# Performance work log

Hardware: AMD Instinct MI355X
Metric: run time of the kernel (lower is better)

## Reference

```python
import jax, jax.numpy as jnp
import numpy as np

N_NODES = 50000
IN_CH = 256
HID_CH = 64
N_EDGES = 800000


def setup_inputs() -> dict:
    key = jax.random.key(0)
    k1, k2, k3, k4, k5 = jax.random.split(key, 5)
    x = jax.random.normal(k1, (N_NODES, IN_CH), dtype=jnp.float32)
    edge_index = jax.random.randint(k2, (2, N_EDGES), 0, N_NODES, dtype=jnp.int64)
    # GCNConv linear weight (Glorot) and zero bias, as in PyG defaults
    W = jax.random.normal(k3, (IN_CH, HID_CH), dtype=jnp.float32) * (1.0 / np.sqrt(IN_CH))
    bias = jnp.zeros((HID_CH,), dtype=jnp.float32)
    # PReLU per-channel weight, torch default init 0.25
    prelu_a = jnp.full((HID_CH,), 0.25, dtype=jnp.float32)
    return {"x": x, "edge_index": edge_index, "W": W, "bias": bias, "prelu_a": prelu_a}


def reference(x, edge_index, W, bias, prelu_a):
    # GCNConv, normalize=False: transform then scatter-add over edges, + bias
    xw = x @ W                               # [N, H]
    src, dst = edge_index[0], edge_index[1]
    msgs = xw[src]                           # [E, H] gather
    agg = jax.ops.segment_sum(msgs, dst, num_segments=N_NODES)  # [N, H]
    out = agg + bias
    # per-channel PReLU
    return jnp.where(out > 0, out, prelu_a * out)
```

## Files before the change

### kernel.cpp

```cpp
#include <hip/hip_runtime.h>

#define N_NODES 50000
#define IN_CH   256
#define HID_CH  64
#define N_EDGES 800000

#define AG_ROWS 64
#define NBUCKET 782
#define CAPB    1536
#define PTILE   4096
#define NPT     196
#define GEMM_BLOCKS 391
#define CAP     2048

typedef __attribute__((ext_vector_type(8))) short short8;
typedef __attribute__((ext_vector_type(4))) float f32x4;

static __device__ __forceinline__ float bf2f(unsigned short h) {
    return __uint_as_float(((unsigned int)h) << 16);
}
static __device__ __forceinline__ unsigned int cvt_pk(float lo, float hi) {
    unsigned int r;
    asm("v_cvt_pk_bf16_f32 %0, %1, %2" : "=v"(r) : "v"(lo), "v"(hi));
    return r;
}

union SmemU {
    short8 wfl[2048];
    struct {
        int hcnt[NBUCKET];
        int excl[NBUCKET];
        int lcur[NBUCKET];
        int gbase[NBUCKET];
        int wsum[8];
        unsigned int staged[PTILE];
        unsigned short sbkt[PTILE];
    } p;
};

__global__ __launch_bounds__(512, 4) void gemm_part_kernel(const float* __restrict__ x,
                                                           const float* __restrict__ W,
                                                           unsigned short* __restrict__ xwb,
                                                           const int* __restrict__ ei,
                                                           int* __restrict__ cnt,
                                                           unsigned int* __restrict__ packed_out) {
    __shared__ SmemU u;
    const int t = threadIdx.x;
    const int bid = blockIdx.x;

    int pid = -1, gid = -1;
    if ((bid & 1) && (bid >> 1) < NPT) pid = bid >> 1;
    else gid = (bid < 2 * NPT) ? (bid >> 1) : (bid - NPT);

    if (gid >= 0) {
        for (int e = t; e < 2048; e += 512) {
            const int ks = e >> 8;
            const int nt = (e >> 6) & 3;
            const int l  = e & 63;
            const int q = l >> 4, m = l & 15;
            const int n = nt * 16 + m;
            const int k0 = ks * 32 + q * 8;
            const float* wp = W + (size_t)k0 * HID_CH + n;
            uint4 v;
            v.x = cvt_pk(wp[0 * HID_CH], wp[1 * HID_CH]);
            v.y = cvt_pk(wp[2 * HID_CH], wp[3 * HID_CH]);
            v.z = cvt_pk(wp[4 * HID_CH], wp[5 * HID_CH]);
            v.w = cvt_pk(wp[6 * HID_CH], wp[7 * HID_CH]);
            ((uint4*)u.wfl)[e] = v;
        }
        __syncthreads();

        const int wv = t >> 6, lane = t & 63;
        const int q = lane >> 4, m = lane & 15;
        const int row0 = gid * 128 + wv * 16;
        const int arow = row0 + m;
        const int arl = arow < N_NODES ? arow : N_NODES - 1;
        const float* xr = x + (size_t)arl * IN_CH + q * 8;

        float4 areg[16];
        #pragma unroll
        for (int ks = 0; ks < 8; ++ks) {
            areg[2 * ks]     = *(const float4*)(xr + ks * 32);
            areg[2 * ks + 1] = *(const float4*)(xr + ks * 32 + 4);
        }

        f32x4 acc0 = {0.f,0.f,0.f,0.f}, acc1 = acc0, acc2 = acc0, acc3 = acc0;

        #pragma unroll
        for (int ks = 0; ks < 8; ++ks) {
            short8 af;
            unsigned int* afu = (unsigned int*)&af;
            afu[0] = cvt_pk(areg[2 * ks].x,     areg[2 * ks].y);
            afu[1] = cvt_pk(areg[2 * ks].z,     areg[2 * ks].w);
            afu[2] = cvt_pk(areg[2 * ks + 1].x, areg[2 * ks + 1].y);
            afu[3] = cvt_pk(areg[2 * ks + 1].z, areg[2 * ks + 1].w);
            const short8 b0 = u.wfl[(ks * 4 + 0) * 64 + lane];
            const short8 b1 = u.wfl[(ks * 4 + 1) * 64 + lane];
            const short8 b2 = u.wfl[(ks * 4 + 2) * 64 + lane];
            const short8 b3 = u.wfl[(ks * 4 + 3) * 64 + lane];
            acc0 = __builtin_amdgcn_mfma_f32_16x16x32_bf16(af, b0, acc0, 0, 0, 0);
            acc1 = __builtin_amdgcn_mfma_f32_16x16x32_bf16(af, b1, acc1, 0, 0, 0);
            acc2 = __builtin_amdgcn_mfma_f32_16x16x32_bf16(af, b2, acc2, 0, 0, 0);
            acc3 = __builtin_amdgcn_mfma_f32_16x16x32_bf16(af, b3, acc3, 0, 0, 0);
        }

        #pragma unroll
        for (int r = 0; r < 4; ++r) {
            const int row = row0 + q * 4 + r;
            if (row < N_NODES) {
                unsigned short* o = xwb + (size_t)row * HID_CH + m;
                const unsigned int p01 = cvt_pk(acc0[r], acc1[r]);
                const unsigned int p23 = cvt_pk(acc2[r], acc3[r]);
                o[0]  = (unsigned short)(p01 & 0xFFFFu);
                o[16] = (unsigned short)(p01 >> 16);
                o[32] = (unsigned short)(p23 & 0xFFFFu);
                o[48] = (unsigned short)(p23 >> 16);
            }
        }
        return;
    }

    const int tile0 = pid * PTILE;
    const int tcnt = min(PTILE, N_EDGES - tile0);

    for (int i = t; i < NBUCKET; i += 512) u.p.hcnt[i] = 0;
    __syncthreads();

    int es[8], ed[8];
    #pragma unroll
    for (int r = 0; r < 2; ++r) {
        const int base = tile0 + (r * 512 + t) * 4;
        if (base < N_EDGES) {
            const int4 s4 = *(const int4*)(ei + base);
            const int4 d4 = *(const int4*)(ei + N_EDGES + base);
            es[r*4+0] = s4.x; es[r*4+1] = s4.y; es[r*4+2] = s4.z; es[r*4+3] = s4.w;
            ed[r*4+0] = d4.x; ed[r*4+1] = d4.y; ed[r*4+2] = d4.z; ed[r*4+3] = d4.w;
        } else {
            #pragma unroll
            for (int j = 0; j < 4; ++j) es[r*4+j] = -1;
        }
    }
    #pragma unroll
    for (int i = 0; i < 8; ++i)
        if (es[i] >= 0) atomicAdd(&u.p.hcnt[ed[i] >> 6], 1);
    __syncthreads();

    const int b0 = 2 * t, b1 = 2 * t + 1;
    const int c0 = (b0 < NBUCKET) ? u.p.hcnt[b0] : 0;
    const int c1 = (b1 < NBUCKET) ? u.p.hcnt[b1] : 0;
    const int v = c0 + c1;
    int s = v;
    #pragma unroll
    for (int off = 1; off < 64; off <<= 1) {
        const int uu = __shfl_up(s, off, 64);
        if ((t & 63) >= off) s += uu;
    }
    if ((t & 63) == 63) u.p.wsum[t >> 6] = s;
    __syncthreads();
    if (t < 8) {
        const int ws = u.p.wsum[t];
        int si = ws;
        #pragma unroll
        for (int off = 1; off < 8; off <<= 1) {
            const int uu = __shfl_up(si, off, 64);
            if (t >= off) si += uu;
        }
        u.p.wsum[t] = si - ws;
    }
    __syncthreads();
    const int ex = s - v + u.p.wsum[t >> 6];
    if (b0 < NBUCKET) {
        u.p.excl[b0] = ex; u.p.lcur[b0] = ex;
        if (c0 > 0) u.p.gbase[b0] = b0 * CAPB + atomicAdd(&cnt[b0], c0);
    }
    if (b1 < NBUCKET) {
        u.p.excl[b1] = ex + c0; u.p.lcur[b1] = ex + c0;
        if (c1 > 0) u.p.gbase[b1] = b1 * CAPB + atomicAdd(&cnt[b1], c1);
    }
    __syncthreads();

    #pragma unroll
    for (int i = 0; i < 8; ++i) {
        if (es[i] >= 0) {
            const int b = ed[i] >> 6;
            const int pos = atomicAdd(&u.p.lcur[b], 1);
            u.p.staged[pos] = ((unsigned int)(ed[i] & 63) << 16) | (unsigned int)es[i];
            u.p.sbkt[pos] = (unsigned short)b;
        }
    }
    __syncthreads();

    #pragma unroll
    for (int i = 0; i < 8; ++i) {
        const int idx = t + i * 512;
        if (idx < tcnt) {
            const int b = u.p.sbkt[idx];
            packed_out[u.p.gbase[b] + (idx - u.p.excl[b])] = u.p.staged[idx];
        }
    }
}

__global__ __launch_bounds__(512) void aggregate_kernel(const unsigned short* __restrict__ xwb,
                                                        const unsigned int* __restrict__ packed,
                                                        const int* __restrict__ cnt,
                                                        const float* __restrict__ bias,
                                                        const float* __restrict__ prelu_a,
                                                        float* __restrict__ out) {
    __shared__ unsigned short ssrc[CAP];
    __shared__ int hcnt[AG_ROWS];
    __shared__ int hexcl[AG_ROWS];
    __shared__ int hcur[AG_ROWS];

    const int b = blockIdx.x;
    const int t = threadIdx.x;
    const int beg = b * CAPB;
    const int total = min(cnt[b], CAP);

    if (t < AG_ROWS) hcnt[t] = 0;
    __syncthreads();

    for (int i = t; i < total; i += 512)
        atomicAdd(&hcnt[packed[beg + i] >> 16], 1);
    __syncthreads();

    if (t < AG_ROWS) {
        const int v = hcnt[t];
        int s = v;
        #pragma unroll
        for (int off = 1; off < 64; off <<= 1) {
            const int u = __shfl_up(s, off, 64);
            if (t >= off) s += u;
        }
        hexcl[t] = s - v;
        hcur[t]  = s - v;
    }
    __syncthreads();

    for (int i = t; i < total; i += 512) {
        const unsigned int p = packed[beg + i];
        const int pos = atomicAdd(&hcur[p >> 16], 1);
        ssrc[pos] = (unsigned short)(p & 0xFFFFu);
    }
    __syncthreads();

    const int sl = t >> 3;
    const int li = t & 7;
    const int c0 = li * 8;
    const int rb = hexcl[sl];
    const int re = rb + hcnt[sl];

    float a[8];
    #pragma unroll
    for (int j = 0; j < 8; ++j) a[j] = 0.f;

    int i = rb;
    for (; i + 7 < re; i += 8) {
        short8 vv[8];
        #pragma unroll
        for (int r = 0; r < 8; ++r) {
            const int e = ssrc[i + r];
            vv[r] = *(const short8*)(xwb + (size_t)e * HID_CH + c0);
        }
        #pragma unroll
        for (int r = 0; r < 8; ++r)
            #pragma unroll
            for (int j = 0; j < 8; ++j)
                a[j] += bf2f((unsigned short)vv[r][j]);
    }
    for (; i + 3 < re; i += 4) {
        short8 vv[4];
        #pragma unroll
        for (int r = 0; r < 4; ++r) {
            const int e = ssrc[i + r];
            vv[r] = *(const short8*)(xwb + (size_t)e * HID_CH + c0);
        }
        #pragma unroll
        for (int r = 0; r < 4; ++r)
            #pragma unroll
            for (int j = 0; j < 8; ++j)
                a[j] += bf2f((unsigned short)vv[r][j]);
    }
    for (; i < re; ++i) {
        const int e0 = ssrc[i];
        const short8 v0 = *(const short8*)(xwb + (size_t)e0 * HID_CH + c0);
        #pragma unroll
        for (int j = 0; j < 8; ++j) a[j] += bf2f((unsigned short)v0[j]);
    }

    const int node = b * AG_ROWS + sl;
    if (node < N_NODES) {
        const float4 bb0 = *(const float4*)(bias + c0);
        const float4 bb1 = *(const float4*)(bias + c0 + 4);
        const float4 aa0 = *(const float4*)(prelu_a + c0);
        const float4 aa1 = *(const float4*)(prelu_a + c0 + 4);
        float4 r0, r1;
        r0.x = a[0] + bb0.x; r0.x = r0.x > 0.f ? r0.x : aa0.x * r0.x;
        r0.y = a[1] + bb0.y; r0.y = r0.y > 0.f ? r0.y : aa0.y * r0.y;
        r0.z = a[2] + bb0.z; r0.z = r0.z > 0.f ? r0.z : aa0.z * r0.z;
        r0.w = a[3] + bb0.w; r0.w = r0.w > 0.f ? r0.w : aa0.w * r0.w;
        r1.x = a[4] + bb1.x; r1.x = r1.x > 0.f ? r1.x : aa1.x * r1.x;
        r1.y = a[5] + bb1.y; r1.y = r1.y > 0.f ? r1.y : aa1.y * r1.y;
        r1.z = a[6] + bb1.z; r1.z = r1.z > 0.f ? r1.z : aa1.z * r1.z;
        r1.w = a[7] + bb1.w; r1.w = r1.w > 0.f ? r1.w : aa1.w * r1.w;
        float4* op = (float4*)(out + (size_t)node * HID_CH + c0);
        op[0] = r0;
        op[1] = r1;
    }
}

extern "C" void kernel_launch(void* const* d_in, const int* in_sizes, int n_in,
                              void* d_out, int out_size, void* d_ws, size_t ws_size,
                              hipStream_t stream) {
    const float* x       = (const float*)d_in[0];
    const int*   ei      = (const int*)d_in[1];
    const float* W       = (const float*)d_in[2];
    const float* bias    = (const float*)d_in[3];
    const float* prelu_a = (const float*)d_in[4];
    float* out = (float*)d_out;

    char* w = (char*)d_ws;
    unsigned short* xwb    = (unsigned short*)(w);
    int*            cnt    = (int*)(w + 6400000);
    unsigned int*   packed = (unsigned int*)(w + 6403200);

    hipMemsetAsync(cnt, 0, NBUCKET * sizeof(int), stream);

    gemm_part_kernel<<<GEMM_BLOCKS + NPT, 512, 0, stream>>>(x, W, xwb, ei, cnt, packed);

    aggregate_kernel<<<NBUCKET, 512, 0, stream>>>(xwb, packed, cnt, bias, prelu_a, out);
}
```

Baseline: 125.2 us.

## Stream GEMM x tiles through double-buffered LDS via async global_load_lds

Replaces the per-thread register preload of the full x row slice with a double-buffered LDS pipeline. It loads 32-column chunks of a 128-row tile using global_load_lds and prefetches the next chunk while computing MFMAs on the current one. The goal is to cut register pressure and overlap global loads with compute. In exchange it adds a block-wide barrier per K step and doubles the shared-memory union size to 64KB. That larger footprint can lower occupancy for both GEMM and partition blocks.

```diff
diff --git a/kernel.cpp b/kernel.cpp
--- a/kernel.cpp
+++ b/kernel.cpp
@@ -12,6 +12,7 @@
 #define NPT     196
 #define GEMM_BLOCKS 391
 #define CAP     2048
+#define XCH     32
 
 typedef __attribute__((ext_vector_type(8))) short short8;
 typedef __attribute__((ext_vector_type(4))) float f32x4;
@@ -24,9 +25,17 @@
     asm("v_cvt_pk_bf16_f32 %0, %1, %2" : "=v"(r) : "v"(lo), "v"(hi));
     return r;
 }
+typedef const __attribute__((address_space(1))) unsigned int* gas_ptr;
+typedef __attribute__((address_space(3))) unsigned int* las_ptr;
+static __device__ __forceinline__ void gl2lds16(const float* g, float* l) {
+    __builtin_amdgcn_global_load_lds((gas_ptr)(g), (las_ptr)(l), 16, 0, 0);
+}
 
 union SmemU {
-    short8 wfl[2048];
+    struct {
+        short8 wfl[2048];
+        float  xs[2][128 * XCH];
+    } g;
     struct {
         int hcnt[NBUCKET];
         int excl[NBUCKET];
@@ -53,60 +62,81 @@
     else gid = (bid < 2 * NPT) ? (bid >> 1) : (bid - NPT);
 
     if (gid >= 0) {
+        const int wv = t >> 6, lane = t & 63;
+        const int q = lane >> 4, m = lane & 15;
+        const int row0 = gid * 128;
+
+        {
+            #pragma unroll
+            for (int r = 0; r < 2; ++r) {
+                const int i = r * 512 + t;
+                const int row = i >> 3;
+                const int grow = min(row0 + row, N_NODES - 1);
+                const float* gp = x + (size_t)grow * IN_CH + 0 * XCH + (i & 7) * 4;
+                float* lp = &u.g.xs[0][(r * 512 + wv * 64) * 4];
+                gl2lds16(gp, lp);
+            }
+        }
+
         for (int e = t; e < 2048; e += 512) {
             const int ks = e >> 8;
             const int nt = (e >> 6) & 3;
             const int l  = e & 63;
-            const int q = l >> 4, m = l & 15;
-            const int n = nt * 16 + m;
-            const int k0 = ks * 32 + q * 8;
+            const int ql = l >> 4, ml = l & 15;
+            const int n = nt * 16 + ml;
+            const int k0 = ks * 32 + ql * 8;
             const float* wp = W + (size_t)k0 * HID_CH + n;
             uint4 v;
             v.x = cvt_pk(wp[0 * HID_CH], wp[1 * HID_CH]);
             v.y = cvt_pk(wp[2 * HID_CH], wp[3 * HID_CH]);
             v.z = cvt_pk(wp[4 * HID_CH], wp[5 * HID_CH]);
             v.w = cvt_pk(wp[6 * HID_CH], wp[7 * HID_CH]);
-            ((uint4*)u.wfl)[e] = v;
+            ((uint4*)u.g.wfl)[e] = v;
         }
         __syncthreads();
 
-        const int wv = t >> 6, lane = t & 63;
-        const int q = lane >> 4, m = lane & 15;
-        const int row0 = gid * 128 + wv * 16;
-        const int arow = row0 + m;
-        const int arl = arow < N_NODES ? arow : N_NODES - 1;
-        const float* xr = x + (size_t)arl * IN_CH + q * 8;
-
-        float4 areg[16];
-        #pragma unroll
-        for (int ks = 0; ks < 8; ++ks) {
-            areg[2 * ks]     = *(const float4*)(xr + ks * 32);
-            areg[2 * ks + 1] = *(const float4*)(xr + ks * 32 + 4);
-        }
-
         f32x4 acc0 = {0.f,0.f,0.f,0.f}, acc1 = acc0, acc2 = acc0, acc3 = acc0;
 
         #pragma unroll
-        for (int ks = 0; ks < 8; ++ks) {
+        for (int kc = 0; kc < 8; ++kc) {
+            const int cur = kc & 1;
+            if (kc < 7) {
+                #pragma unroll
+                for (int r = 0; r < 2; ++r) {
+                    const int i = r * 512 + t;
+                    const int row = i >> 3;
+                    const int grow = min(row0 + row, N_NODES - 1);
+                    const float* gp = x + (size_t)grow * IN_CH + (kc + 1) * XCH + (i & 7) * 4;
+                    float* lp = &u.g.xs[cur ^ 1][(r * 512 + wv * 64) * 4];
+                    gl2lds16(gp, lp);
+                }
+            }
+
+            const float* ap = &u.g.xs[cur][(wv * 16 + m) * XCH + q * 8];
+            const float4 a0 = *(const float4*)ap;
+            const float4 a1 = *(const float4*)(ap + 4);
             short8 af;
             unsigned int* afu = (unsigned int*)&af;
-            afu[0] = cvt_pk(areg[2 * ks].x,     areg[2 * ks].y);
-            afu[1] = cvt_pk(areg[2 * ks].z,     areg[2 * ks].w);
-            afu[2] = cvt_pk(areg[2 * ks + 1].x, areg[2 * ks + 1].y);
-            afu[3] = cvt_pk(areg[2 * ks + 1].z, areg[2 * ks + 1].w);
-            const short8 b0 = u.wfl[(ks * 4 + 0) * 64 + lane];
-            const short8 b1 = u.wfl[(ks * 4 + 1) * 64 + lane];
-            const short8 b2 = u.wfl[(ks * 4 + 2) * 64 + lane];
-            const short8 b3 = u.wfl[(ks * 4 + 3) * 64 + lane];
+            afu[0] = cvt_pk(a0.x, a0.y);
+            afu[1] = cvt_pk(a0.z, a0.w);
+            afu[2] = cvt_pk(a1.x, a1.y);
+            afu[3] = cvt_pk(a1.z, a1.w);
+            const short8 b0 = u.g.wfl[(kc * 4 + 0) * 64 + lane];
+            const short8 b1 = u.g.wfl[(kc * 4 + 1) * 64 + lane];
+            const short8 b2 = u.g.wfl[(kc * 4 + 2) * 64 + lane];
+            const short8 b3 = u.g.wfl[(kc * 4 + 3) * 64 + lane];
             acc0 = __builtin_amdgcn_mfma_f32_16x16x32_bf16(af, b0, acc0, 0, 0, 0);
             acc1 = __builtin_amdgcn_mfma_f32_16x16x32_bf16(af, b1, acc1, 0, 0, 0);
             acc2 = __builtin_amdgcn_mfma_f32_16x16x32_bf16(af, b2, acc2, 0, 0, 0);
             acc3 = __builtin_amdgcn_mfma_f32_16x16x32_bf16(af, b3, acc3, 0, 0, 0);
-        }
-
+
+            if (kc < 7) __syncthreads();
+        }
+
+        const int rowt = row0 + wv * 16;
         #pragma unroll
         for (int r = 0; r < 4; ++r) {
-            const int row = row0 + q * 4 + r;
+            const int row = rowt + q * 4 + r;
             if (row < N_NODES) {
                 unsigned short* o = xwb + (size_t)row * HID_CH + m;
                 const unsigned int p01 = cvt_pk(acc0[r], acc1[r]);
```

New measurement: 126.7 us. Within noise of the previous version (+1.3%).

## Fuse GEMM/partition and aggregation into one cooperative persistent kernel

Applied to the files above, without the earlier changes.

Merges the two kernels into a single cooperative kernel that loops over GEMM and partition work items, does a grid-wide sync, then loops over aggregation buckets. The aim is to drop the second kernel launch and the gap between dependent launches. In exchange the grid is capped (at most 512 blocks) and work is serialized within persistent blocks. The grid barrier also adds its own cost, and the shared-memory union grows to hold the aggregation buffers.

```diff
diff --git a/kernel.cpp b/kernel.cpp
--- a/kernel.cpp
+++ b/kernel.cpp
@@ -1,4 +1,5 @@
 #include <hip/hip_runtime.h>
+#include <hip/hip_cooperative_groups.h>
 
 #define N_NODES 50000
 #define IN_CH   256
@@ -11,6 +12,7 @@
 #define PTILE   4096
 #define NPT     196
 #define GEMM_BLOCKS 391
+#define NITEMS  (GEMM_BLOCKS + NPT)
 #define CAP     2048
 
 typedef __attribute__((ext_vector_type(8))) short short8;
@@ -36,90 +38,90 @@
         unsigned int staged[PTILE];
         unsigned short sbkt[PTILE];
     } p;
+    struct {
+        unsigned short ssrc[CAP];
+        int hcnt[AG_ROWS];
+        int hexcl[AG_ROWS];
+        int hcur[AG_ROWS];
+    } a;
 };
 
-__global__ __launch_bounds__(512, 4) void gemm_part_kernel(const float* __restrict__ x,
-                                                           const float* __restrict__ W,
-                                                           unsigned short* __restrict__ xwb,
-                                                           const int* __restrict__ ei,
-                                                           int* __restrict__ cnt,
-                                                           unsigned int* __restrict__ packed_out) {
-    __shared__ SmemU u;
-    const int t = threadIdx.x;
-    const int bid = blockIdx.x;
-
-    int pid = -1, gid = -1;
-    if ((bid & 1) && (bid >> 1) < NPT) pid = bid >> 1;
-    else gid = (bid < 2 * NPT) ? (bid >> 1) : (bid - NPT);
-
-    if (gid >= 0) {
-        for (int e = t; e < 2048; e += 512) {
-            const int ks = e >> 8;
-            const int nt = (e >> 6) & 3;
-            const int l  = e & 63;
-            const int q = l >> 4, m = l & 15;
-            const int n = nt * 16 + m;
-            const int k0 = ks * 32 + q * 8;
-            const float* wp = W + (size_t)k0 * HID_CH + n;
-            uint4 v;
-            v.x = cvt_pk(wp[0 * HID_CH], wp[1 * HID_CH]);
-            v.y = cvt_pk(wp[2 * HID_CH], wp[3 * HID_CH]);
-            v.z = cvt_pk(wp[4 * HID_CH], wp[5 * HID_CH]);
-            v.w = cvt_pk(wp[6 * HID_CH], wp[7 * HID_CH]);
-            ((uint4*)u.wfl)[e] = v;
-        }
-        __syncthreads();
-
-        const int wv = t >> 6, lane = t & 63;
-        const int q = lane >> 4, m = lane & 15;
-        const int row0 = gid * 128 + wv * 16;
-        const int arow = row0 + m;
-        const int arl = arow < N_NODES ? arow : N_NODES - 1;
-        const float* xr = x + (size_t)arl * IN_CH + q * 8;
-
-        float4 areg[16];
-        #pragma unroll
-        for (int ks = 0; ks < 8; ++ks) {
-            areg[2 * ks]     = *(const float4*)(xr + ks * 32);
-            areg[2 * ks + 1] = *(const float4*)(xr + ks * 32 + 4);
-        }
-
-        f32x4 acc0 = {0.f,0.f,0.f,0.f}, acc1 = acc0, acc2 = acc0, acc3 = acc0;
-
-        #pragma unroll
-        for (int ks = 0; ks < 8; ++ks) {
-            short8 af;
-            unsigned int* afu = (unsigned int*)&af;
-            afu[0] = cvt_pk(areg[2 * ks].x,     areg[2 * ks].y);
-            afu[1] = cvt_pk(areg[2 * ks].z,     areg[2 * ks].w);
-            afu[2] = cvt_pk(areg[2 * ks + 1].x, areg[2 * ks + 1].y);
-            afu[3] = cvt_pk(areg[2 * ks + 1].z, areg[2 * ks + 1].w);
-            const short8 b0 = u.wfl[(ks * 4 + 0) * 64 + lane];
-            const short8 b1 = u.wfl[(ks * 4 + 1) * 64 + lane];
-            const short8 b2 = u.wfl[(ks * 4 + 2) * 64 + lane];
-            const short8 b3 = u.wfl[(ks * 4 + 3) * 64 + lane];
-            acc0 = __builtin_amdgcn_mfma_f32_16x16x32_bf16(af, b0, acc0, 0, 0, 0);
-            acc1 = __builtin_amdgcn_mfma_f32_16x16x32_bf16(af, b1, acc1, 0, 0, 0);
-            acc2 = __builtin_amdgcn_mfma_f32_16x16x32_bf16(af, b2, acc2, 0, 0, 0);
-            acc3 = __builtin_amdgcn_mfma_f32_16x16x32_bf16(af, b3, acc3, 0, 0, 0);
-        }
-
-        #pragma unroll
-        for (int r = 0; r < 4; ++r) {
-            const int row = row0 + q * 4 + r;
-            if (row < N_NODES) {
-                unsigned short* o = xwb + (size_t)row * HID_CH + m;
-                const unsigned int p01 = cvt_pk(acc0[r], acc1[r]);
-                const unsigned int p23 = cvt_pk(acc2[r], acc3[r]);
-                o[0]  = (unsigned short)(p01 & 0xFFFFu);
-                o[16] = (unsigned short)(p01 >> 16);
-                o[32] = (unsigned short)(p23 & 0xFFFFu);
-                o[48] = (unsigned short)(p23 >> 16);
-            }
-        }
-        return;
-    }
-
+static __device__ __forceinline__ void gemm_role(int gid, SmemU& u,
+                                                 const float* __restrict__ x,
+                                                 const float* __restrict__ W,
+                                                 unsigned short* __restrict__ xwb,
+                                                 int t) {
+    for (int e = t; e < 2048; e += 512) {
+        const int ks = e >> 8;
+        const int nt = (e >> 6) & 3;
+        const int l  = e & 63;
+        const int ql = l >> 4, ml = l & 15;
+        const int n = nt * 16 + ml;
+        const int k0 = ks * 32 + ql * 8;
+        const float* wp = W + (size_t)k0 * HID_CH + n;
+        uint4 v;
+        v.x = cvt_pk(wp[0 * HID_CH], wp[1 * HID_CH]);
+        v.y = cvt_pk(wp[2 * HID_CH], wp[3 * HID_CH]);
+        v.z = cvt_pk(wp[4 * HID_CH], wp[5 * HID_CH]);
+        v.w = cvt_pk(wp[6 * HID_CH], wp[7 * HID_CH]);
+        ((uint4*)u.wfl)[e] = v;
+    }
+    __syncthreads();
+
+    const int wv = t >> 6, lane = t & 63;
+    const int q = lane >> 4, m = lane & 15;
+    const int row0 = gid * 128 + wv * 16;
+    const int arow = row0 + m;
+    const int arl = arow < N_NODES ? arow : N_NODES - 1;
+    const float* xr = x + (size_t)arl * IN_CH + q * 8;
+
+    float4 areg[16];
+    #pragma unroll
+    for (int ks = 0; ks < 8; ++ks) {
+        areg[2 * ks]     = *(const float4*)(xr + ks * 32);
+        areg[2 * ks + 1] = *(const float4*)(xr + ks * 32 + 4);
+    }
+
+    f32x4 acc0 = {0.f,0.f,0.f,0.f}, acc1 = acc0, acc2 = acc0, acc3 = acc0;
+
+    #pragma unroll
+    for (int ks = 0; ks < 8; ++ks) {
+        short8 af;
+        unsigned int* afu = (unsigned int*)&af;
+        afu[0] = cvt_pk(areg[2 * ks].x,     areg[2 * ks].y);
+        afu[1] = cvt_pk(areg[2 * ks].z,     areg[2 * ks].w);
+        afu[2] = cvt_pk(areg[2 * ks + 1].x, areg[2 * ks + 1].y);
+        afu[3] = cvt_pk(areg[2 * ks + 1].z, areg[2 * ks + 1].w);
+        const short8 b0 = u.wfl[(ks * 4 + 0) * 64 + lane];
+        const short8 b1 = u.wfl[(ks * 4 + 1) * 64 + lane];
+        const short8 b2 = u.wfl[(ks * 4 + 2) * 64 + lane];
+        const short8 b3 = u.wfl[(ks * 4 + 3) * 64 + lane];
+        acc0 = __builtin_amdgcn_mfma_f32_16x16x32_bf16(af, b0, acc0, 0, 0, 0);
+        acc1 = __builtin_amdgcn_mfma_f32_16x16x32_bf16(af, b1, acc1, 0, 0, 0);
+        acc2 = __builtin_amdgcn_mfma_f32_16x16x32_bf16(af, b2, acc2, 0, 0, 0);
+        acc3 = __builtin_amdgcn_mfma_f32_16x16x32_bf16(af, b3, acc3, 0, 0, 0);
+    }
+
+    #pragma unroll
+    for (int r = 0; r < 4; ++r) {
+        const int row = row0 + q * 4 + r;
+        if (row < N_NODES) {
+            unsigned short* o = xwb + (size_t)row * HID_CH + m;
+            const unsigned int p01 = cvt_pk(acc0[r], acc1[r]);
+            const unsigned int p23 = cvt_pk(acc2[r], acc3[r]);
+            o[0]  = (unsigned short)(p01 & 0xFFFFu);
+            o[16] = (unsigned short)(p01 >> 16);
+            o[32] = (unsigned short)(p23 & 0xFFFFu);
+            o[48] = (unsigned short)(p23 >> 16);
+        }
+    }
+}
+
+static __device__ __forceinline__ void part_role(int pid, SmemU& u,
+                                                 const int* __restrict__ ei,
+                                                 int* __restrict__ cnt,
+                                                 unsigned int* __restrict__ packed_out,
+                                                 int t) {
     const int tile0 = pid * PTILE;
     const int tcnt = min(PTILE, N_EDGES - tile0);
 
@@ -200,54 +202,49 @@
     }
 }
 
-__global__ __launch_bounds__(512) void aggregate_kernel(const unsigned short* __restrict__ xwb,
-                                                        const unsigned int* __restrict__ packed,
-                                                        const int* __restrict__ cnt,
-                                                        const float* __restrict__ bias,
-                                                        const float* __restrict__ prelu_a,
-                                                        float* __restrict__ out) {
-    __shared__ unsigned short ssrc[CAP];
-    __shared__ int hcnt[AG_ROWS];
-    __shared__ int hexcl[AG_ROWS];
-    __shared__ int hcur[AG_ROWS];
-
-    const int b = blockIdx.x;
-    const int t = threadIdx.x;
+static __device__ __forceinline__ void agg_role(int b, SmemU& u,
+                                                const unsigned short* __restrict__ xwb,
+                                                const unsigned int* __restrict__ packed,
+                                                const int* __restrict__ cnt,
+                                                const float* __restrict__ bias,
+                                                const float* __restrict__ prelu_a,
+                                                float* __restrict__ out,
+                                                int t) {
     const int beg = b * CAPB;
     const int total = min(cnt[b], CAP);
 
-    if (t < AG_ROWS) hcnt[t] = 0;
+    if (t < AG_ROWS) u.a.hcnt[t] = 0;
     __syncthreads();
 
     for (int i = t; i < total; i += 512)
-        atomicAdd(&hcnt[packed[beg + i] >> 16], 1);
+        atomicAdd(&u.a.hcnt[packed[beg + i] >> 16], 1);
     __syncthreads();
 
     if (t < AG_ROWS) {
-        const int v = hcnt[t];
+        const int v = u.a.hcnt[t];
         int s = v;
         #pragma unroll
         for (int off = 1; off < 64; off <<= 1) {
-            const int u = __shfl_up(s, off, 64);
-            if (t >= off) s += u;
-        }
-        hexcl[t] = s - v;
-        hcur[t]  = s - v;
+            const int uu = __shfl_up(s, off, 64);
+            if (t >= off) s += uu;
+        }
+        u.a.hexcl[t] = s - v;
+        u.a.hcur[t]  = s - v;
     }
     __syncthreads();
 
     for (int i = t; i < total; i += 512) {
         const unsigned int p = packed[beg + i];
-        const int pos = atomicAdd(&hcur[p >> 16], 1);
-        ssrc[pos] = (unsigned short)(p & 0xFFFFu);
+        const int pos = atomicAdd(&u.a.hcur[p >> 16], 1);
+        u.a.ssrc[pos] = (unsigned short)(p & 0xFFFFu);
     }
     __syncthreads();
 
     const int sl = t >> 3;
     const int li = t & 7;
     const int c0 = li * 8;
-    const int rb = hexcl[sl];
-    const int re = rb + hcnt[sl];
+    const int rb = u.a.hexcl[sl];
+    const int re = rb + u.a.hcnt[sl];
 
     float a[8];
     #pragma unroll
@@ -258,7 +255,7 @@
         short8 vv[8];
         #pragma unroll
         for (int r = 0; r < 8; ++r) {
-            const int e = ssrc[i + r];
+            const int e = u.a.ssrc[i + r];
             vv[r] = *(const short8*)(xwb + (size_t)e * HID_CH + c0);
         }
         #pragma unroll
@@ -271,7 +268,7 @@
         short8 vv[4];
         #pragma unroll
         for (int r = 0; r < 4; ++r) {
-            const int e = ssrc[i + r];
+            const int e = u.a.ssrc[i + r];
             vv[r] = *(const short8*)(xwb + (size_t)e * HID_CH + c0);
         }
         #pragma unroll
@@ -281,7 +278,7 @@
                 a[j] += bf2f((unsigned short)vv[r][j]);
     }
     for (; i < re; ++i) {
-        const int e0 = ssrc[i];
+        const int e0 = u.a.ssrc[i];
         const short8 v0 = *(const short8*)(xwb + (size_t)e0 * HID_CH + c0);
         #pragma unroll
         for (int j = 0; j < 8; ++j) a[j] += bf2f((unsigned short)v0[j]);
@@ -308,6 +305,33 @@
     }
 }
 
+__global__ __launch_bounds__(512, 4) void fused_kernel(const float* __restrict__ x,
+                                                       const float* __restrict__ W,
+                                                       unsigned short* __restrict__ xwb,
+                                                       const int* __restrict__ ei,
+                                                       int* __restrict__ cnt,
+                                                       unsigned int* __restrict__ packed,
+                                                       const float* __restrict__ bias,
+                                                       const float* __restrict__ prelu_a,
+                                                       float* __restrict__ out) {
+    __shared__ SmemU u;
+    const int t = threadIdx.x;
+    const int nb = gridDim.x;
+
+    for (int item = blockIdx.x; item < NITEMS; item += nb) {
+        if (item < GEMM_BLOCKS) gemm_role(item, u, x, W, xwb, t);
+        else                    part_role(item - GEMM_BLOCKS, u, ei, cnt, packed, t);
+        __syncthreads();
+    }
+
+    cooperative_groups::this_grid().sync();
+
+    for (int b = blockIdx.x; b < NBUCKET; b += nb) {
+        agg_role(b, u, xwb, packed, cnt, bias, prelu_a, out, t);
+        __syncthreads();
+    }
+}
+
 extern "C" void kernel_launch(void* const* d_in, const int* in_sizes, int n_in,
                               void* d_out, int out_size, void* d_ws, size_t ws_size,
                               hipStream_t stream) {
@@ -323,9 +347,20 @@
     int*            cnt    = (int*)(w + 6400000);
     unsigned int*   packed = (unsigned int*)(w + 6403200);
 
+    static int nblk = 0;
+    if (nblk == 0) {
+        int perCU = 0;
+        if (hipOccupancyMaxActiveBlocksPerMultiprocessor(&perCU, fused_kernel, 512, 0)
+                != hipSuccess || perCU <= 0)
+            perCU = 1;
+        nblk = perCU * 256;
+        if (nblk > 512) nblk = 512;
+    }
+
     hipMemsetAsync(cnt, 0, NBUCKET * sizeof(int), stream);
 
-    gemm_part_kernel<<<GEMM_BLOCKS + NPT, 512, 0, stream>>>(x, W, xwb, ei, cnt, packed);
-
-    aggregate_kernel<<<NBUCKET, 512, 0, stream>>>(xwb, packed, cnt, bias, prelu_a, out);
-}
+    void* args[] = {(void*)&x, (void*)&W, (void*)&xwb, (void*)&ei, (void*)&cnt,
+                    (void*)&packed, (void*)&bias, (void*)&prelu_a, (void*)&out};
+    hipLaunchCooperativeKernel((void*)fused_kernel, dim3(nblk), dim3(512),
+                               args, 0, stream);
+}
```

Result: slower. 195.9 us (+56.5%).
